# Optimization experiments

Measured on AMD Instinct MI355X. Metric: run time of the kernel, lower is better.

## Reference

```python
import jax, jax.numpy as jnp
import numpy as np

N = 50000   # nodes
E = 600000  # directed edges
B = 128     # graphs
IN = 128
H = 128
K = 30      # sort-pool k
C_OUT = 32
KER = 5
OUT_DIM = 10
L_OUT = K - KER + 1  # 26


def setup_inputs() -> dict:
    key = jax.random.key(0)
    ks = jax.random.split(key, 12)
    s = 0.05
    return {
        "x": jax.random.normal(ks[0], (N, IN), jnp.float32),
        "edge_index": jax.random.randint(ks[1], (2, E), 0, N),
        "batch": jnp.sort(jax.random.randint(ks[2], (N,), 0, B)),
        "W0": jax.random.normal(ks[3], (IN, H), jnp.float32) * s,
        "b0": jnp.zeros((H,), jnp.float32),
        "W1": jax.random.normal(ks[4], (H, H), jnp.float32) * s,
        "b1": jnp.zeros((H,), jnp.float32),
        "W2": jax.random.normal(ks[5], (H, H), jnp.float32) * s,
        "b2": jnp.zeros((H,), jnp.float32),
        "conv_w": jax.random.normal(ks[6], (C_OUT, H, KER), jnp.float32) * s,
        "conv_b": jnp.zeros((C_OUT,), jnp.float32),
        "lin1_w": jax.random.normal(ks[7], (C_OUT * L_OUT, H), jnp.float32) * s,
        "lin1_b": jnp.zeros((H,), jnp.float32),
        "lin2_w": jax.random.normal(ks[8], (H, OUT_DIM), jnp.float32) * s,
        "lin2_b": jnp.zeros((OUT_DIM,), jnp.float32),
    }


def reference(x, edge_index, batch, W0, b0, W1, b1, W2, b2,
              conv_w, conv_b, lin1_w, lin1_b, lin2_w, lin2_b):
    # --- GCN normalization (A + I, symmetric deg^-1/2) ---
    loops = jnp.arange(N)
    row = jnp.concatenate([edge_index[0], loops])  # source
    col = jnp.concatenate([edge_index[1], loops])  # target (aggregation side)
    deg = jax.ops.segment_sum(jnp.ones_like(col, dtype=x.dtype), col, num_segments=N)
    dinv = jax.lax.rsqrt(jnp.maximum(deg, 1.0))
    norm = dinv[row] * dinv[col]  # [E+N]

    def gcn(h, W, b):
        hw = h @ W                                            # [N,H]
        msg = hw[row] * norm[:, None]                         # gather [E+N,H]
        return jax.ops.segment_sum(msg, col, num_segments=N) + b

    h = jax.nn.relu(gcn(x, W0, b0))
    h = jax.nn.relu(gcn(h, W1, b1))
    h = jax.nn.relu(gcn(h, W2, b2))

    # --- SortAggregation: per-graph sort by last channel (desc), top-K, zero-pad ---
    last = h[:, -1]
    order = jnp.lexsort((-last, batch))  # primary: batch, secondary: last desc
    hs = h[order]
    bs = batch[order]
    counts = jax.ops.segment_sum(jnp.ones((N,), jnp.int32), batch, num_segments=B)
    starts = jnp.cumsum(counts) - counts  # exclusive prefix sum
    rank = jnp.arange(N) - starts[bs]     # within-graph rank after sort
    r = jnp.where(rank < K, rank, K)      # overflow bucket K is discarded
    pooled = jnp.zeros((B, K + 1, H), h.dtype).at[bs, r].add(hs)[:, :K]  # [B,K,H]

    # --- conv1d head (NCH layout, matches torch view/transpose) ---
    xc = jnp.transpose(pooled, (0, 2, 1))  # [B,H,K]
    y = jax.lax.conv_general_dilated(xc, conv_w, (1,), "VALID",
                                     dimension_numbers=("NCH", "OIH", "NCH"))
    y = jax.nn.relu(y + conv_b[None, :, None])  # [B,C_OUT,L_OUT]
    y = y.reshape(B, -1)
    y = jax.nn.relu(y @ lin1_w + lin1_b)
    return y @ lin2_w + lin2_b  # [B,OUT_DIM]
```

## Files before the change

kernel.cpp:

```cpp
#include <hip/hip_runtime.h>
#include <math.h>

#define Nn 50000
#define Ee 600000
#define Bg 128
#define Hd 128
#define Kt 30
#define CO 32
#define KW 5
#define LOUT 26
#define CAP 2048
#define SCB 196
#define MMB 782

typedef float v2f __attribute__((ext_vector_type(2)));
typedef short bf16x8 __attribute__((ext_vector_type(8)));
typedef float f32x4 __attribute__((ext_vector_type(4)));

__device__ __forceinline__ unsigned short bfr(float v) {
    unsigned u = __builtin_bit_cast(unsigned, v);
    unsigned r = (u + 0x7FFFu + ((u >> 16) & 1u)) >> 16;
    return (unsigned short)r;
}
__device__ __forceinline__ float bff(unsigned short h) {
    unsigned u = ((unsigned)h) << 16;
    return __builtin_bit_cast(float, u);
}

__global__ void countpack_kernel(const int* __restrict__ ei, const int* __restrict__ batch,
                            int* __restrict__ deg_i, int* __restrict__ bstart,
                            const float* __restrict__ conv_w, float* __restrict__ wT2,
                            const float* __restrict__ W0, const float* __restrict__ W1,
                            const float* __restrict__ W2,
                            ushort* __restrict__ Bph, ushort* __restrict__ Bpm,
                            ushort* __restrict__ Bpl) {
    int i = blockIdx.x * 256 + threadIdx.x;
    if (i < Ee) atomicAdd(&deg_i[ei[Ee + i]], 1);
    if (i < Nn) {
        int b = batch[i];
        if (i == 0) bstart[b] = 0;
        else if (batch[i - 1] != b) bstart[b] = i;
    }
    if (i == 0) bstart[Bg] = Nn;
    if (i < CO * KW * Hd) {
        int ci = i & 127;
        int r = i >> 7;
        int o = r / KW, k = r - o * KW;
        wT2[i] = conv_w[((size_t)o * Hd + ci) * KW + k];
    }
    if (i < 3 * 2048) {
        int l = i >> 11;
        int r = i & 2047;
        int kc = r >> 9;
        int n = (r >> 6) & 7;
        int lane = r & 63;
        int m = lane & 15, kq = lane >> 4;
        const float* W = (l == 0) ? W0 : (l == 1) ? W1 : W2;
        int col = n * 16 + m;
        size_t off = ((size_t)l * 2048 + (size_t)((kc * 8 + n) * 64 + lane)) * 8;
#pragma unroll
        for (int j = 0; j < 8; ++j) {
            float v = W[(size_t)(kc * 32 + kq * 8 + j) * Hd + col];
            unsigned short h = bfr(v);
            float r1 = v - bff(h);
            unsigned short mid = bfr(r1);
            Bph[off + j] = h;
            Bpm[off + j] = mid;
            Bpl[off + j] = bfr(r1 - bff(mid));
        }
    }
}

__global__ __launch_bounds__(256) void scanBC2_kernel(const int* __restrict__ deg_i,
                            int* __restrict__ row_ptr, float* __restrict__ dinv,
                            int* __restrict__ bstart) {
    __shared__ int ls[256];
    __shared__ int boffS;
    int tid = threadIdx.x;
    int b = blockIdx.x;
    int s = 0;
    for (int k = 0; k < b; ++k)
        s += deg_i[k * 256 + tid] + 1;
    ls[tid] = s;
    __syncthreads();
    for (int off = 128; off > 0; off >>= 1) {
        if (tid < off) ls[tid] += ls[tid + off];
        __syncthreads();
    }
    if (tid == 0) boffS = ls[0];
    __syncthreads();
    int boff = boffS;
    int i = b * 256 + tid;
    int v2 = 0;
    if (i < Nn) {
        int raw = deg_i[i];
        v2 = raw + 1;
        dinv[i] = 1.0f / sqrtf((float)(raw + 2));
    }
    ls[tid] = v2;
    __syncthreads();
    for (int off = 1; off < 256; off <<= 1) {
        int t = (tid >= off) ? ls[tid - off] : 0;
        __syncthreads();
        ls[tid] += t;
        __syncthreads();
    }
    if (i < Nn) row_ptr[i + 1] = ls[tid] + boff;
    if (i == 0) row_ptr[0] = 0;
    if (b == 0 && tid == 0) {
        for (int bb = Bg - 1; bb >= 0; --bb)
            if (bstart[bb] == -1) bstart[bb] = bstart[bb + 1];
    }
}

__device__ __forceinline__ void mmx_body(int bid, int tid,
                            const float* __restrict__ Hin,
                            const ushort* __restrict__ Bph, const ushort* __restrict__ Bpm,
                            const ushort* __restrict__ Bpl,
                            const float* __restrict__ dinv, float* __restrict__ hw) {
    int w = tid >> 6, lane = tid & 63;
    int m = lane & 15, kq = lane >> 4;
    int rowA = bid * 64 + w * 16 + m;
    bool va = rowA < Nn;
    const float* ap = Hin + (size_t)rowA * Hd;
    f32x4 acc[8];
#pragma unroll
    for (int n = 0; n < 8; ++n) acc[n] = (f32x4)0.f;
#pragma unroll
    for (int kc = 0; kc < 4; ++kc) {
        bf16x8 a0 = (bf16x8)0, a1 = (bf16x8)0, a2 = (bf16x8)0;
        if (va) {
            float av[8];
            *(float4*)&av[0] = *(const float4*)(ap + kc * 32 + kq * 8);
            *(float4*)&av[4] = *(const float4*)(ap + kc * 32 + kq * 8 + 4);
#pragma unroll
            for (int j = 0; j < 8; ++j) {
                unsigned short h = bfr(av[j]);
                float r1 = av[j] - bff(h);
                unsigned short mid = bfr(r1);
                a0[j] = (short)h;
                a1[j] = (short)mid;
                a2[j] = (short)bfr(r1 - bff(mid));
            }
        }
        const ushort* bhp = Bph + (size_t)((kc * 8) * 64 + lane) * 8;
        const ushort* bmp = Bpm + (size_t)((kc * 8) * 64 + lane) * 8;
        const ushort* blp = Bpl + (size_t)((kc * 8) * 64 + lane) * 8;
#pragma unroll
        for (int n = 0; n < 8; ++n) {
            bf16x8 b0 = *(const bf16x8*)(bhp + (size_t)n * 64 * 8);
            bf16x8 b1 = *(const bf16x8*)(bmp + (size_t)n * 64 * 8);
            bf16x8 b2 = *(const bf16x8*)(blp + (size_t)n * 64 * 8);
            acc[n] = __builtin_amdgcn_mfma_f32_16x16x32_bf16(a0, b0, acc[n], 0, 0, 0);
            acc[n] = __builtin_amdgcn_mfma_f32_16x16x32_bf16(a1, b0, acc[n], 0, 0, 0);
            acc[n] = __builtin_amdgcn_mfma_f32_16x16x32_bf16(a0, b1, acc[n], 0, 0, 0);
            acc[n] = __builtin_amdgcn_mfma_f32_16x16x32_bf16(a1, b1, acc[n], 0, 0, 0);
            acc[n] = __builtin_amdgcn_mfma_f32_16x16x32_bf16(a2, b0, acc[n], 0, 0, 0);
            acc[n] = __builtin_amdgcn_mfma_f32_16x16x32_bf16(a0, b2, acc[n], 0, 0, 0);
        }
    }
    int rbase = bid * 64 + w * 16 + kq * 4;
#pragma unroll
    for (int reg = 0; reg < 4; ++reg) {
        int r = rbase + reg;
        if (r < Nn) {
            float s = dinv[r];
#pragma unroll
            for (int n = 0; n < 8; ++n)
                hw[(size_t)r * Hd + n * 16 + m] = acc[n][reg] * s;
        }
    }
}

__global__ __launch_bounds__(256) void mmx_kernel(const float* __restrict__ Hin,
                            const ushort* __restrict__ Bph, const ushort* __restrict__ Bpm,
                            const ushort* __restrict__ Bpl,
                            const float* __restrict__ dinv, float* __restrict__ hw) {
    mmx_body(blockIdx.x, threadIdx.x, Hin, Bph, Bpm, Bpl, dinv, hw);
}

__global__ __launch_bounds__(256) void mmxfill_kernel(const float* __restrict__ Hin,
                            const ushort* __restrict__ Bph, const ushort* __restrict__ Bpm,
                            const ushort* __restrict__ Bpl,
                            const float* __restrict__ dinv, float* __restrict__ hw,
                            const int* __restrict__ ei, const int* __restrict__ row_ptr,
                            int* __restrict__ cnt, int* __restrict__ csr_src) {
    if (blockIdx.x < MMB) {
        mmx_body(blockIdx.x, threadIdx.x, Hin, Bph, Bpm, Bpl, dinv, hw);
    } else {
        int e = (blockIdx.x - MMB) * 256 + threadIdx.x;
        if (e < Ee) {
            int c = ei[Ee + e];
            int r = ei[e];
            int p = row_ptr[c] + atomicAdd(&cnt[c], 1) + 1;
            csr_src[p] = r;
        }
    }
}

__global__ __launch_bounds__(256) void agg_kernel(const float* __restrict__ hw,
                            const int* __restrict__ row_ptr, const int* __restrict__ csr_src,
                            const float* __restrict__ dinv, const float* __restrict__ bias,
                            float* __restrict__ hout) {
    int node = blockIdx.x * 4 + (threadIdx.x >> 6);
    if (node >= Nn) return;
    int lane = threadIdx.x & 63;
    const v2f* hw2 = (const v2f*)hw;
    v2f a0 = hw2[(size_t)node * 64 + lane];
    v2f a1 = 0.f, a2 = 0.f, a3 = 0.f;
    v2f a4 = 0.f, a5 = 0.f, a6 = 0.f, a7 = 0.f;
    int e0 = row_ptr[node], e1 = row_ptr[node + 1];
    int e = e0;
    for (; e + 7 < e1; e += 8) {
        int s0 = __builtin_nontemporal_load(csr_src + e);
        int s1 = __builtin_nontemporal_load(csr_src + e + 1);
        int s2 = __builtin_nontemporal_load(csr_src + e + 2);
        int s3 = __builtin_nontemporal_load(csr_src + e + 3);
        int s4 = __builtin_nontemporal_load(csr_src + e + 4);
        int s5 = __builtin_nontemporal_load(csr_src + e + 5);
        int s6 = __builtin_nontemporal_load(csr_src + e + 6);
        int s7 = __builtin_nontemporal_load(csr_src + e + 7);
        a0 += hw2[(size_t)s0 * 64 + lane];
        a1 += hw2[(size_t)s1 * 64 + lane];
        a2 += hw2[(size_t)s2 * 64 + lane];
        a3 += hw2[(size_t)s3 * 64 + lane];
        a4 += hw2[(size_t)s4 * 64 + lane];
        a5 += hw2[(size_t)s5 * 64 + lane];
        a6 += hw2[(size_t)s6 * 64 + lane];
        a7 += hw2[(size_t)s7 * 64 + lane];
    }
    if (e + 3 < e1) {
        int s0 = __builtin_nontemporal_load(csr_src + e);
        int s1 = __builtin_nontemporal_load(csr_src + e + 1);
        int s2 = __builtin_nontemporal_load(csr_src + e + 2);
        int s3 = __builtin_nontemporal_load(csr_src + e + 3);
        a4 += hw2[(size_t)s0 * 64 + lane];
        a5 += hw2[(size_t)s1 * 64 + lane];
        a6 += hw2[(size_t)s2 * 64 + lane];
        a7 += hw2[(size_t)s3 * 64 + lane];
        e += 4;
    }
    for (; e < e1; ++e) {
        int s0 = __builtin_nontemporal_load(csr_src + e);
        a0 += hw2[(size_t)s0 * 64 + lane];
    }
    v2f acc = ((a0 + a1) + (a2 + a3)) + ((a4 + a5) + (a6 + a7));
    float d = dinv[node];
    v2f bv = ((const v2f*)bias)[lane];
    v2f o;
    o.x = fmaxf(fmaf(d, acc.x, bv.x), 0.f);
    o.y = fmaxf(fmaf(d, acc.y, bv.y), 0.f);
    ((v2f*)hout)[(size_t)node * 64 + lane] = o;
}

__global__ __launch_bounds__(256) void lastcol_kernel(const float* __restrict__ hw,
                            const int* __restrict__ row_ptr, const int* __restrict__ csr_src,
                            const float* __restrict__ dinv, const float* __restrict__ b2,
                            float* __restrict__ lastv) {
    int node = blockIdx.x * 256 + threadIdx.x;
    if (node >= Nn) return;
    float a0 = hw[(size_t)node * Hd + 127];
    float a1 = 0.f, a2 = 0.f, a3 = 0.f, a4 = 0.f, a5 = 0.f, a6 = 0.f, a7 = 0.f;
    int e0 = row_ptr[node], e1 = row_ptr[node + 1];
    int e = e0;
    for (; e + 7 < e1; e += 8) {
        int s0 = __builtin_nontemporal_load(csr_src + e);
        int s1 = __builtin_nontemporal_load(csr_src + e + 1);
        int s2 = __builtin_nontemporal_load(csr_src + e + 2);
        int s3 = __builtin_nontemporal_load(csr_src + e + 3);
        int s4 = __builtin_nontemporal_load(csr_src + e + 4);
        int s5 = __builtin_nontemporal_load(csr_src + e + 5);
        int s6 = __builtin_nontemporal_load(csr_src + e + 6);
        int s7 = __builtin_nontemporal_load(csr_src + e + 7);
        a0 += hw[(size_t)s0 * Hd + 127];
        a1 += hw[(size_t)s1 * Hd + 127];
        a2 += hw[(size_t)s2 * Hd + 127];
        a3 += hw[(size_t)s3 * Hd + 127];
        a4 += hw[(size_t)s4 * Hd + 127];
        a5 += hw[(size_t)s5 * Hd + 127];
        a6 += hw[(size_t)s6 * Hd + 127];
        a7 += hw[(size_t)s7 * Hd + 127];
    }
    if (e + 3 < e1) {
        int s0 = __builtin_nontemporal_load(csr_src + e);
        int s1 = __builtin_nontemporal_load(csr_src + e + 1);
        int s2 = __builtin_nontemporal_load(csr_src + e + 2);
        int s3 = __builtin_nontemporal_load(csr_src + e + 3);
        a4 += hw[(size_t)s0 * Hd + 127];
        a5 += hw[(size_t)s1 * Hd + 127];
        a6 += hw[(size_t)s2 * Hd + 127];
        a7 += hw[(size_t)s3 * Hd + 127];
        e += 4;
    }
    for (; e < e1; ++e) {
        int s0 = __builtin_nontemporal_load(csr_src + e);
        a0 += hw[(size_t)s0 * Hd + 127];
    }
    float acc = ((a0 + a1) + (a2 + a3)) + ((a4 + a5) + (a6 + a7));
    lastv[node] = fmaxf(fmaf(dinv[node], acc, b2[127]), 0.f);
}

__global__ __launch_bounds__(1024) void tail_kernel(const float* __restrict__ hw,
                            const int* __restrict__ bstart, const int* __restrict__ row_ptr,
                            const int* __restrict__ csr_src, const float* __restrict__ dinv,
                            const float* __restrict__ b2, const float* __restrict__ lastv,
                            const float* __restrict__ wT2, const float* __restrict__ conv_b,
                            const float* __restrict__ l1w, const float* __restrict__ l1b,
                            const float* __restrict__ l2w, const float* __restrict__ l2b,
                            float* __restrict__ out) {
    __shared__ float vals[CAP];
    __shared__ float xcl[Kt][130];
    __shared__ float fl[CO * LOUT];
    __shared__ float pz[8][Hd];
    __shared__ float z[Hd];
    __shared__ int selS[Kt];
    int b = blockIdx.x, tid = threadIdx.x;

    int s0 = bstart[b], s1 = bstart[b + 1];
    int n = s1 - s0;
    int nc = n < CAP ? n : CAP;
    if (tid < Kt) selS[tid] = -1;
    for (int j = tid; j < nc; j += 1024)
        vals[j] = lastv[s0 + j];
    __syncthreads();

    for (int j = tid; j < nc; j += 1024) {
        float vj = vals[j];
        int rank = 0;
        for (int i = 0; i < nc; ++i) {
            float vi = vals[i];
            rank += (vi > vj || (vi == vj && i < j)) ? 1 : 0;
        }
        if (rank < Kt) selS[rank] = s0 + j;
    }
    __syncthreads();

    int wv = tid >> 6, lane = tid & 63;
    const v2f* hw2 = (const v2f*)hw;
    v2f bv = ((const v2f*)b2)[lane];
    for (int t = wv; t < Kt; t += 16) {
        int s = selS[t];
        v2f o = (v2f)0.f;
        if (s >= 0) {
            v2f a0 = hw2[(size_t)s * 64 + lane];
            v2f a1 = 0.f, a2 = 0.f, a3 = 0.f;
            v2f a4 = 0.f, a5 = 0.f, a6 = 0.f, a7 = 0.f;
            int e0 = row_ptr[s], e1 = row_ptr[s + 1];
            int e = e0;
            for (; e + 7 < e1; e += 8) {
                int q0 = __builtin_nontemporal_load(csr_src + e);
                int q1 = __builtin_nontemporal_load(csr_src + e + 1);
                int q2 = __builtin_nontemporal_load(csr_src + e + 2);
                int q3 = __builtin_nontemporal_load(csr_src + e + 3);
                int q4 = __builtin_nontemporal_load(csr_src + e + 4);
                int q5 = __builtin_nontemporal_load(csr_src + e + 5);
                int q6 = __builtin_nontemporal_load(csr_src + e + 6);
                int q7 = __builtin_nontemporal_load(csr_src + e + 7);
                a0 += hw2[(size_t)q0 * 64 + lane];
                a1 += hw2[(size_t)q1 * 64 + lane];
                a2 += hw2[(size_t)q2 * 64 + lane];
                a3 += hw2[(size_t)q3 * 64 + lane];
                a4 += hw2[(size_t)q4 * 64 + lane];
                a5 += hw2[(size_t)q5 * 64 + lane];
                a6 += hw2[(size_t)q6 * 64 + lane];
                a7 += hw2[(size_t)q7 * 64 + lane];
            }
            if (e + 3 < e1) {
                int q0 = __builtin_nontemporal_load(csr_src + e);
                int q1 = __builtin_nontemporal_load(csr_src + e + 1);
                int q2 = __builtin_nontemporal_load(csr_src + e + 2);
                int q3 = __builtin_nontemporal_load(csr_src + e + 3);
                a4 += hw2[(size_t)q0 * 64 + lane];
                a5 += hw2[(size_t)q1 * 64 + lane];
                a6 += hw2[(size_t)q2 * 64 + lane];
                a7 += hw2[(size_t)q3 * 64 + lane];
                e += 4;
            }
            for (; e < e1; ++e) {
                int q0 = __builtin_nontemporal_load(csr_src + e);
                a0 += hw2[(size_t)q0 * 64 + lane];
            }
            v2f acc = ((a0 + a1) + (a2 + a3)) + ((a4 + a5) + (a6 + a7));
            float d = dinv[s];
            o.x = fmaxf(fmaf(d, acc.x, bv.x), 0.f);
            o.y = fmaxf(fmaf(d, acc.y, bv.y), 0.f);
        }
        xcl[t][lane * 2] = o.x;
        xcl[t][lane * 2 + 1] = o.y;
    }
    __syncthreads();
    if (tid < CO * LOUT) {
        int o = tid / LOUT, t = tid - o * LOUT;
        float acc = conv_b[o];
#pragma unroll
        for (int k = 0; k < KW; ++k) {
            const float* xr = &xcl[t + k][0];
            const float* wr = wT2 + ((size_t)o * KW + k) * Hd;
#pragma unroll 8
            for (int c4 = 0; c4 < 32; ++c4) {
                float2 xa = *(const float2*)(xr + c4 * 4);
                float2 xb = *(const float2*)(xr + c4 * 4 + 2);
                float4 wv2 = *(const float4*)(wr + c4 * 4);
                acc = fmaf(xa.x, wv2.x, acc);
                acc = fmaf(xa.y, wv2.y, acc);
                acc = fmaf(xb.x, wv2.z, acc);
                acc = fmaf(xb.y, wv2.w, acc);
            }
        }
        fl[tid] = fmaxf(acc, 0.f);
    }
    __syncthreads();
    int hh = tid & 127, chunk = tid >> 7;
    int m0 = chunk * 104;
    float acc = 0.f;
    const float* lw = l1w + (size_t)m0 * Hd + hh;
#pragma unroll 8
    for (int m = 0; m < 104; ++m)
        acc = fmaf(fl[m0 + m], lw[(size_t)m * Hd], acc);
    pz[chunk][hh] = acc;
    __syncthreads();
    if (tid < Hd) {
        float a = l1b[tid];
#pragma unroll
        for (int q = 0; q < 8; ++q) a += pz[q][tid];
        z[tid] = fmaxf(a, 0.f);
    }
    __syncthreads();
    if (tid < 10) {
        float a2 = l2b[tid];
        for (int j = 0; j < Hd; ++j)
            a2 = fmaf(z[j], l2w[j * 10 + tid], a2);
        out[b * 10 + tid] = a2;
    }
}

extern "C" void kernel_launch(void* const* d_in, const int* in_sizes, int n_in,
                              void* d_out, int out_size, void* d_ws, size_t ws_size,
                              hipStream_t stream) {
    const float* x      = (const float*)d_in[0];
    const int*   ei     = (const int*)d_in[1];
    const int*   batch  = (const int*)d_in[2];
    const float* W0     = (const float*)d_in[3];
    const float* b0     = (const float*)d_in[4];
    const float* W1     = (const float*)d_in[5];
    const float* b1     = (const float*)d_in[6];
    const float* W2     = (const float*)d_in[7];
    const float* b2     = (const float*)d_in[8];
    const float* conv_w = (const float*)d_in[9];
    const float* conv_b = (const float*)d_in[10];
    const float* l1w    = (const float*)d_in[11];
    const float* l1b    = (const float*)d_in[12];
    const float* l2w    = (const float*)d_in[13];
    const float* l2b    = (const float*)d_in[14];
    float* out = (float*)d_out;

    int* wsI = (int*)d_ws;
    size_t off = 0;
    int*   deg_i   = wsI + off; off += Nn;
    int*   cnt     = wsI + off; off += Nn;
    int*   bstart  = wsI + off; off += 132;
    int*   row_ptr = wsI + off; off += 50004;
    float* dinv    = (float*)(wsI + off); off += Nn;
    int*   csr_src = wsI + off; off += Ee;
    off = (off + 3) & ~(size_t)3;
    ushort* Bph  = (ushort*)(wsI + off); off += 3 * 16384 / 2;
    ushort* Bpm  = (ushort*)(wsI + off); off += 3 * 16384 / 2;
    ushort* Bpl  = (ushort*)(wsI + off); off += 3 * 16384 / 2;
    float* hw    = (float*)(wsI + off); off += (size_t)Nn * Hd;
    float* hbuf  = (float*)(wsI + off); off += (size_t)Nn * Hd;
    float* wT2   = (float*)(wsI + off); off += CO * KW * Hd;
    float* lastv = (float*)(wsI + off); off += Nn;

    hipMemsetAsync(deg_i, 0xFF, (size_t)(Nn + Nn + 132) * 4, stream);
    countpack_kernel<<<(Ee + 255) / 256, 256, 0, stream>>>(ei, batch, deg_i, bstart,
        conv_w, wT2, W0, W1, W2, Bph, Bpm, Bpl);
    scanBC2_kernel<<<SCB, 256, 0, stream>>>(deg_i, row_ptr, dinv, bstart);
    dim3 aggGrid((Nn + 3) / 4);
    mmxfill_kernel<<<MMB + (Ee + 255) / 256, 256, 0, stream>>>(x, Bph, Bpm, Bpl,
        dinv, hw, ei, row_ptr, cnt, csr_src);
    agg_kernel<<<aggGrid, 256, 0, stream>>>(hw, row_ptr, csr_src, dinv, b0, hbuf);
    mmx_kernel<<<MMB, 256, 0, stream>>>(hbuf, Bph + 16384, Bpm + 16384, Bpl + 16384, dinv, hw);
    agg_kernel<<<aggGrid, 256, 0, stream>>>(hw, row_ptr, csr_src, dinv, b1, hbuf);
    mmx_kernel<<<MMB, 256, 0, stream>>>(hbuf, Bph + 32768, Bpm + 32768, Bpl + 32768, dinv, hw);
    lastcol_kernel<<<(Nn + 255) / 256, 256, 0, stream>>>(hw, row_ptr, csr_src, dinv, b2, lastv);
    tail_kernel<<<Bg, 1024, 0, stream>>>(hw, bstart, row_ptr, csr_src, dinv, b2, lastv,
                                         wT2, conv_b, l1w, l1b, l2w, l2b, out);
}
```

Before: 403.8 us.

## Fuse last-column aggregation into tail kernel and stage A tile through LDS

Removes the separate lastcol kernel and its lastv buffer by computing each graph's last-channel aggregation inside the tail kernel, one block per graph. This saves a launch and a global round trip. In exchange that gather now runs on only 128 blocks instead of a full grid. Separately, the mmx GEMM body now loads its 64x128 A tile into shared memory with coalesced float4 loads before splitting it into bf16 parts, replacing the strided per-lane global reads but adding a barrier and about 33KB of LDS per block.

After: 398.8 us. About the same (-1.2%).

```diff
diff --git a/kernel.cpp b/kernel.cpp
--- a/kernel.cpp
+++ b/kernel.cpp
@@ -118,30 +118,40 @@
                             const ushort* __restrict__ Bph, const ushort* __restrict__ Bpm,
                             const ushort* __restrict__ Bpl,
                             const float* __restrict__ dinv, float* __restrict__ hw) {
+    __shared__ __align__(16) float At[64][132];
     int w = tid >> 6, lane = tid & 63;
     int m = lane & 15, kq = lane >> 4;
-    int rowA = bid * 64 + w * 16 + m;
-    bool va = rowA < Nn;
-    const float* ap = Hin + (size_t)rowA * Hd;
+    {
+        const f32x4* g4 = (const f32x4*)(Hin + (size_t)bid * 64 * Hd);
+        int rowsLeft = Nn - bid * 64;
+#pragma unroll
+        for (int i = 0; i < 8; ++i) {
+            int f = i * 256 + tid;
+            int r = f >> 5, c4 = f & 31;
+            f32x4 v = (f32x4)0.f;
+            if (r < rowsLeft) v = g4[f];
+            *(f32x4*)&At[r][c4 * 4] = v;
+        }
+    }
+    __syncthreads();
+    const float* arow = &At[w * 16 + m][0];
     f32x4 acc[8];
 #pragma unroll
     for (int n = 0; n < 8; ++n) acc[n] = (f32x4)0.f;
 #pragma unroll
     for (int kc = 0; kc < 4; ++kc) {
-        bf16x8 a0 = (bf16x8)0, a1 = (bf16x8)0, a2 = (bf16x8)0;
-        if (va) {
-            float av[8];
-            *(float4*)&av[0] = *(const float4*)(ap + kc * 32 + kq * 8);
-            *(float4*)&av[4] = *(const float4*)(ap + kc * 32 + kq * 8 + 4);
-#pragma unroll
-            for (int j = 0; j < 8; ++j) {
-                unsigned short h = bfr(av[j]);
-                float r1 = av[j] - bff(h);
-                unsigned short mid = bfr(r1);
-                a0[j] = (short)h;
-                a1[j] = (short)mid;
-                a2[j] = (short)bfr(r1 - bff(mid));
-            }
+        bf16x8 a0, a1, a2;
+        float av[8];
+        *(f32x4*)&av[0] = *(const f32x4*)(arow + kc * 32 + kq * 8);
+        *(f32x4*)&av[4] = *(const f32x4*)(arow + kc * 32 + kq * 8 + 4);
+#pragma unroll
+        for (int j = 0; j < 8; ++j) {
+            unsigned short h = bfr(av[j]);
+            float r1 = av[j] - bff(h);
+            unsigned short mid = bfr(r1);
+            a0[j] = (short)h;
+            a1[j] = (short)mid;
+            a2[j] = (short)bfr(r1 - bff(mid));
         }
         const ushort* bhp = Bph + (size_t)((kc * 8) * 64 + lane) * 8;
         const ushort* bmp = Bpm + (size_t)((kc * 8) * 64 + lane) * 8;
@@ -253,57 +263,10 @@
     ((v2f*)hout)[(size_t)node * 64 + lane] = o;
 }
 
-__global__ __launch_bounds__(256) void lastcol_kernel(const float* __restrict__ hw,
-                            const int* __restrict__ row_ptr, const int* __restrict__ csr_src,
-                            const float* __restrict__ dinv, const float* __restrict__ b2,
-                            float* __restrict__ lastv) {
-    int node = blockIdx.x * 256 + threadIdx.x;
-    if (node >= Nn) return;
-    float a0 = hw[(size_t)node * Hd + 127];
-    float a1 = 0.f, a2 = 0.f, a3 = 0.f, a4 = 0.f, a5 = 0.f, a6 = 0.f, a7 = 0.f;
-    int e0 = row_ptr[node], e1 = row_ptr[node + 1];
-    int e = e0;
-    for (; e + 7 < e1; e += 8) {
-        int s0 = __builtin_nontemporal_load(csr_src + e);
-        int s1 = __builtin_nontemporal_load(csr_src + e + 1);
-        int s2 = __builtin_nontemporal_load(csr_src + e + 2);
-        int s3 = __builtin_nontemporal_load(csr_src + e + 3);
-        int s4 = __builtin_nontemporal_load(csr_src + e + 4);
-        int s5 = __builtin_nontemporal_load(csr_src + e + 5);
-        int s6 = __builtin_nontemporal_load(csr_src + e + 6);
-        int s7 = __builtin_nontemporal_load(csr_src + e + 7);
-        a0 += hw[(size_t)s0 * Hd + 127];
-        a1 += hw[(size_t)s1 * Hd + 127];
-        a2 += hw[(size_t)s2 * Hd + 127];
-        a3 += hw[(size_t)s3 * Hd + 127];
-        a4 += hw[(size_t)s4 * Hd + 127];
-        a5 += hw[(size_t)s5 * Hd + 127];
-        a6 += hw[(size_t)s6 * Hd + 127];
-        a7 += hw[(size_t)s7 * Hd + 127];
-    }
-    if (e + 3 < e1) {
-        int s0 = __builtin_nontemporal_load(csr_src + e);
-        int s1 = __builtin_nontemporal_load(csr_src + e + 1);
-        int s2 = __builtin_nontemporal_load(csr_src + e + 2);
-        int s3 = __builtin_nontemporal_load(csr_src + e + 3);
-        a4 += hw[(size_t)s0 * Hd + 127];
-        a5 += hw[(size_t)s1 * Hd + 127];
-        a6 += hw[(size_t)s2 * Hd + 127];
-        a7 += hw[(size_t)s3 * Hd + 127];
-        e += 4;
-    }
-    for (; e < e1; ++e) {
-        int s0 = __builtin_nontemporal_load(csr_src + e);
-        a0 += hw[(size_t)s0 * Hd + 127];
-    }
-    float acc = ((a0 + a1) + (a2 + a3)) + ((a4 + a5) + (a6 + a7));
-    lastv[node] = fmaxf(fmaf(dinv[node], acc, b2[127]), 0.f);
-}
-
 __global__ __launch_bounds__(1024) void tail_kernel(const float* __restrict__ hw,
                             const int* __restrict__ bstart, const int* __restrict__ row_ptr,
                             const int* __restrict__ csr_src, const float* __restrict__ dinv,
-                            const float* __restrict__ b2, const float* __restrict__ lastv,
+                            const float* __restrict__ b2,
                             const float* __restrict__ wT2, const float* __restrict__ conv_b,
                             const float* __restrict__ l1w, const float* __restrict__ l1b,
                             const float* __restrict__ l2w, const float* __restrict__ l2b,
@@ -320,8 +283,49 @@
     int n = s1 - s0;
     int nc = n < CAP ? n : CAP;
     if (tid < Kt) selS[tid] = -1;
-    for (int j = tid; j < nc; j += 1024)
-        vals[j] = lastv[s0 + j];
+    float b2l = b2[127];
+    for (int j = tid; j < nc; j += 1024) {
+        int node = s0 + j;
+        float a0 = hw[(size_t)node * Hd + 127];
+        float a1 = 0.f, a2 = 0.f, a3 = 0.f, a4 = 0.f, a5 = 0.f, a6 = 0.f, a7 = 0.f;
+        int e0 = row_ptr[node], e1 = row_ptr[node + 1];
+        int e = e0;
+        for (; e + 7 < e1; e += 8) {
+            int q0 = __builtin_nontemporal_load(csr_src + e);
+            int q1 = __builtin_nontemporal_load(csr_src + e + 1);
+            int q2 = __builtin_nontemporal_load(csr_src + e + 2);
+            int q3 = __builtin_nontemporal_load(csr_src + e + 3);
+            int q4 = __builtin_nontemporal_load(csr_src + e + 4);
+            int q5 = __builtin_nontemporal_load(csr_src + e + 5);
+            int q6 = __builtin_nontemporal_load(csr_src + e + 6);
+            int q7 = __builtin_nontemporal_load(csr_src + e + 7);
+            a0 += hw[(size_t)q0 * Hd + 127];
+            a1 += hw[(size_t)q1 * Hd + 127];
+            a2 += hw[(size_t)q2 * Hd + 127];
+            a3 += hw[(size_t)q3 * Hd + 127];
+            a4 += hw[(size_t)q4 * Hd + 127];
+            a5 += hw[(size_t)q5 * Hd + 127];
+            a6 += hw[(size_t)q6 * Hd + 127];
+            a7 += hw[(size_t)q7 * Hd + 127];
+        }
+        if (e + 3 < e1) {
+            int q0 = __builtin_nontemporal_load(csr_src + e);
+            int q1 = __builtin_nontemporal_load(csr_src + e + 1);
+            int q2 = __builtin_nontemporal_load(csr_src + e + 2);
+            int q3 = __builtin_nontemporal_load(csr_src + e + 3);
+            a4 += hw[(size_t)q0 * Hd + 127];
+            a5 += hw[(size_t)q1 * Hd + 127];
+            a6 += hw[(size_t)q2 * Hd + 127];
+            a7 += hw[(size_t)q3 * Hd + 127];
+            e += 4;
+        }
+        for (; e < e1; ++e) {
+            int q0 = __builtin_nontemporal_load(csr_src + e);
+            a0 += hw[(size_t)q0 * Hd + 127];
+        }
+        float acc = ((a0 + a1) + (a2 + a3)) + ((a4 + a5) + (a6 + a7));
+        vals[j] = fmaxf(fmaf(dinv[node], acc, b2l), 0.f);
+    }
     __syncthreads();
 
     for (int j = tid; j < nc; j += 1024) {
@@ -469,7 +473,6 @@
     float* hw    = (float*)(wsI + off); off += (size_t)Nn * Hd;
     float* hbuf  = (float*)(wsI + off); off += (size_t)Nn * Hd;
     float* wT2   = (float*)(wsI + off); off += CO * KW * Hd;
-    float* lastv = (float*)(wsI + off); off += Nn;
 
     hipMemsetAsync(deg_i, 0xFF, (size_t)(Nn + Nn + 132) * 4, stream);
     countpack_kernel<<<(Ee + 255) / 256, 256, 0, stream>>>(ei, batch, deg_i, bstart,
@@ -482,7 +485,6 @@
     mmx_kernel<<<MMB, 256, 0, stream>>>(hbuf, Bph + 16384, Bpm + 16384, Bpl + 16384, dinv, hw);
     agg_kernel<<<aggGrid, 256, 0, stream>>>(hw, row_ptr, csr_src, dinv, b1, hbuf);
     mmx_kernel<<<MMB, 256, 0, stream>>>(hbuf, Bph + 32768, Bpm + 32768, Bpl + 32768, dinv, hw);
-    lastcol_kernel<<<(Nn + 255) / 256, 256, 0, stream>>>(hw, row_ptr, csr_src, dinv, b2, lastv);
-    tail_kernel<<<Bg, 1024, 0, stream>>>(hw, bstart, row_ptr, csr_src, dinv, b2, lastv,
+    tail_kernel<<<Bg, 1024, 0, stream>>>(hw, bstart, row_ptr, csr_src, dinv, b2,
                                          wT2, conv_b, l1w, l1b, l2w, l2b, out);
 }
```
